# Optimization experiments

Measured on AMD Instinct MI355X. Metric: run time of the kernel, lower is better.

Reference implementation:

```python
import jax, jax.numpy as jnp
import numpy as np

DIM = 256
HEADS = 8
G = 8            # group (window) size per axis
POS_DIM = 16     # (dim // 4) // 4
MLP_HIDDEN = 4 * DIM


def layernorm(x, g, b, eps=1e-5):
    m = x.mean(-1, keepdims=True)
    v = ((x - m) ** 2).mean(-1, keepdims=True)
    return (x - m) / jnp.sqrt(v + eps) * g + b


def setup_inputs() -> dict:
    key = jax.random.key(0)
    ks = jax.random.split(key, 32)
    s = 0.02
    d = {}
    d['x'] = jax.random.normal(ks[0], (1, 32768, DIM), jnp.float32)
    d['y'] = jax.random.normal(ks[1], (1, 32768, DIM), jnp.float32)
    d['n1_g'] = jnp.ones((DIM,), jnp.float32)
    d['n1_b'] = jnp.zeros((DIM,), jnp.float32)
    d['qkv_w'] = jax.random.normal(ks[2], (DIM, 3 * DIM), jnp.float32) * s
    d['qkv_b'] = jnp.zeros((3 * DIM,), jnp.float32)
    d['pp_w'] = jax.random.normal(ks[3], (3, POS_DIM), jnp.float32) * s
    d['pp_b'] = jnp.zeros((POS_DIM,), jnp.float32)
    d['p1_lng'] = jnp.ones((POS_DIM,), jnp.float32)
    d['p1_lnb'] = jnp.zeros((POS_DIM,), jnp.float32)
    d['p1_w'] = jax.random.normal(ks[4], (POS_DIM, POS_DIM), jnp.float32) * s
    d['p1_b'] = jnp.zeros((POS_DIM,), jnp.float32)
    d['p2_lng'] = jnp.ones((POS_DIM,), jnp.float32)
    d['p2_lnb'] = jnp.zeros((POS_DIM,), jnp.float32)
    d['p2_w'] = jax.random.normal(ks[5], (POS_DIM, POS_DIM), jnp.float32) * s
    d['p2_b'] = jnp.zeros((POS_DIM,), jnp.float32)
    d['p3_lng'] = jnp.ones((POS_DIM,), jnp.float32)
    d['p3_lnb'] = jnp.zeros((POS_DIM,), jnp.float32)
    d['p3_w'] = jax.random.normal(ks[6], (POS_DIM, HEADS), jnp.float32) * s
    d['p3_b'] = jnp.zeros((HEADS,), jnp.float32)
    d['proj_w'] = jax.random.normal(ks[7], (DIM, DIM), jnp.float32) * s
    d['proj_b'] = jnp.zeros((DIM,), jnp.float32)
    d['n2_g'] = jnp.ones((DIM,), jnp.float32)
    d['n2_b'] = jnp.zeros((DIM,), jnp.float32)
    d['fc1_w'] = jax.random.normal(ks[8], (DIM, MLP_HIDDEN), jnp.float32) * s
    d['fc1_b'] = jnp.zeros((MLP_HIDDEN,), jnp.float32)
    d['fc2_w'] = jax.random.normal(ks[9], (MLP_HIDDEN, DIM), jnp.float32) * s
    d['fc2_b'] = jnp.zeros((DIM,), jnp.float32)
    d['H'] = 32
    d['W'] = 32
    d['D'] = 32
    return d


def reference(x, y, n1_g, n1_b, qkv_w, qkv_b, pp_w, pp_b,
              p1_lng, p1_lnb, p1_w, p1_b, p2_lng, p2_lnb, p2_w, p2_b,
              p3_lng, p3_lnb, p3_w, p3_b, proj_w, proj_b,
              n2_g, n2_b, fc1_w, fc1_b, fc2_w, fc2_b, H, W, D):
    B, L, C = x.shape
    nh, g = HEADS, G
    hd = C // nh
    shortcut = x
    xn = layernorm(x, n1_g, n1_b)
    xv = xn.reshape(B, H, W, D, C)
    yv = y.reshape(B, H, W, D, C)  # note: y is NOT normed in the original

    # SDA window partition (H,W,D divisible by g -> no padding, zero mask)
    def part(t):
        t = t.reshape(B, H // g, g, W // g, g, D // g, g, C)
        t = t.transpose(0, 1, 3, 5, 2, 4, 6, 7)
        return t.reshape(-1, g * g * g, C)

    xg, yg = part(xv), part(yv)
    B_, N, _ = xg.shape

    # original quirk: self.qkv used for BOTH x and y (qkv_y layer unused)
    qkv = (xg @ qkv_w + qkv_b).reshape(B_, N, 3, nh, hd).transpose(2, 0, 3, 1, 4)
    qkv_y = (yg @ qkv_w + qkv_b).reshape(B_, N, 3, nh, hd).transpose(2, 0, 3, 1, 4)
    q = qkv[0] * (hd ** -0.5)
    k_y, v_y = qkv_y[1], qkv_y[2]

    attn = jnp.einsum('bhnd,bhmd->bhnm', q, k_y)  # [B_, nh, N, N]

    # dynamic relative position bias (small MLP + gather)
    rng = jnp.arange(1 - g, g)
    bh, bw, bd = jnp.meshgrid(rng, rng, rng, indexing='ij')
    biases = jnp.stack([bh, bw, bd], -1).reshape(-1, 3).astype(x.dtype)  # [(2g-1)^3, 3]
    pos = biases @ pp_w + pp_b
    pos = jax.nn.relu(layernorm(pos, p1_lng, p1_lnb)) @ p1_w + p1_b
    pos = jax.nn.relu(layernorm(pos, p2_lng, p2_lnb)) @ p2_w + p2_b
    pos = jax.nn.relu(layernorm(pos, p3_lng, p3_lnb)) @ p3_w + p3_b  # [(2g-1)^3, nh]

    c = jnp.arange(g)
    ch, cw, cd = jnp.meshgrid(c, c, c, indexing='ij')
    cf = jnp.stack([ch, cw, cd], 0).reshape(3, -1)          # [3, g^3]
    rel = (cf[:, :, None] - cf[:, None, :]).transpose(1, 2, 0) + (g - 1)
    idx = rel[..., 0] * (2 * g - 1) * (2 * g - 1) + rel[..., 1] * (2 * g - 1) + rel[..., 2]
    bias = pos[idx].transpose(2, 0, 1)  # [nh, N, N]

    attn = jax.nn.softmax(attn + bias[None], axis=-1)
    out = jnp.einsum('bhnm,bhmd->bhnd', attn, v_y).transpose(0, 2, 1, 3).reshape(B_, N, C)
    out = out @ proj_w + proj_b

    # reverse window partition
    out = out.reshape(B, H // g, W // g, D // g, g, g, g, C)
    out = out.transpose(0, 1, 4, 2, 5, 3, 6, 7).reshape(B, H * W * D, C)

    x = shortcut + out
    x2 = layernorm(x, n2_g, n2_b)
    h = jax.nn.gelu(x2 @ fc1_w + fc1_b, approximate=False)
    x = x + (h @ fc2_w + fc2_b)
    return x
```

## Files before the change

kernel.cpp:

```cpp
#include <hip/hip_runtime.h>
#include <cstdint>
#include <cstddef>

typedef unsigned int u32;
typedef unsigned short u16;
typedef __attribute__((ext_vector_type(8))) short bf16x8;
typedef __attribute__((ext_vector_type(4))) float f32x4;

#define DEV __device__ __forceinline__

DEV u16 f2b(float f){ u32 x = __float_as_uint(f); x += 0x7fffu + ((x>>16)&1u); return (u16)(x>>16); }
DEV u32 pk2(float a, float b){
  u32 r;
  asm("v_cvt_pk_bf16_f32 %0, %1, %2" : "=v"(r) : "v"(a), "v"(b));
  return r;
}

DEV void gll16(const void* g, void* l){
  __builtin_amdgcn_global_load_lds((const __attribute__((address_space(1))) u32*)g,
                                   (__attribute__((address_space(3))) u32*)l, 16, 0, 0);
}

DEV void win_n(int r, int& win, int& n){
  int d_ = r & 31, w_ = (r>>5)&31, h_ = r>>10;
  win = ((h_>>3)<<4) | ((w_>>3)<<2) | (d_>>3);
  n   = ((h_&7)<<6)  | ((w_&7)<<3)  | (d_&7);
}
DEV int tok_of(int r){
  int win = r>>9, nn = r&511;
  int bh = win>>4, bw=(win>>2)&3, bd=win&3;
  int ih = nn>>6,  iw=(nn>>3)&7,  id=nn&7;
  return ((bh*8+ih)<<10) | ((bw*8+iw)<<5) | (bd*8+id);
}


__global__ void wtrall_k(const float* __restrict__ qkv_w, const float* __restrict__ proj_w,
                         const float* __restrict__ fc1_w, const float* __restrict__ fc2_w,
                         u16* __restrict__ qkvT, u16* __restrict__ projT,
                         u16* __restrict__ fc1T, u16* __restrict__ fc2T){
  int f = blockIdx.x*256 + threadIdx.x;
  const float* w; u16* wt; int g; bool k10 = false; int N;
  if (f < 196608)      { w=qkv_w;  wt=qkvT;  g=f;        N=768;  }
  else if (f < 262144) { w=proj_w; wt=projT; g=f-196608; N=256;  }
  else if (f < 524288) { w=fc1_w;  wt=fc1T;  g=f-262144; N=1024; }
  else                 { w=fc2_w;  wt=fc2T;  g=f-524288; N=256;  k10=true; }
  int n = k10 ? (g>>10) : (g>>8);
  int k = k10 ? (g&1023) : (g&255);
  wt[g] = f2b(w[(size_t)k*N + n]);
}

__global__ void conv_k(const float* __restrict__ x, u16* __restrict__ o, int n4){
  int stride = gridDim.x*blockDim.x;
  for (int i = blockIdx.x*blockDim.x + threadIdx.x; i < n4; i += stride){
    const float4 v = *(const float4*)(x + (size_t)i*4);
    u32 lo = (u32)f2b(v.x) | ((u32)f2b(v.y)<<16);
    u32 hi = (u32)f2b(v.z) | ((u32)f2b(v.w)<<16);
    *(uint2*)(o + (size_t)i*4) = make_uint2(lo, hi);
  }
}

__global__ __launch_bounds__(256)
void ln_k(const float* __restrict__ x, const float* __restrict__ g,
          const float* __restrict__ b, u16* __restrict__ out){
  int row  = blockIdx.x*4 + (threadIdx.x>>6);
  int lane = threadIdx.x & 63;
  const float4 v = *(const float4*)(x + (size_t)row*256 + lane*4);
  float s = v.x+v.y+v.z+v.w;
  #pragma unroll
  for (int m=1;m<64;m<<=1) s += __shfl_xor(s, m);
  float mean = s * (1.0f/256.0f);
  float d0=v.x-mean,d1=v.y-mean,d2=v.z-mean,d3=v.w-mean;
  float q = d0*d0+d1*d1+d2*d2+d3*d3;
  #pragma unroll
  for (int m=1;m<64;m<<=1) q += __shfl_xor(q, m);
  float rs = rsqrtf(q*(1.0f/256.0f) + 1e-5f);
  const float4 gg = *(const float4*)(g + lane*4);
  const float4 bb = *(const float4*)(b + lane*4);
  u32 lo = (u32)f2b(d0*rs*gg.x+bb.x) | ((u32)f2b(d1*rs*gg.y+bb.y)<<16);
  u32 hi = (u32)f2b(d2*rs*gg.z+bb.z) | ((u32)f2b(d3*rs*gg.w+bb.w)<<16);
  *(uint2*)(out + (size_t)row*256 + lane*4) = make_uint2(lo,hi);
}

template<int NOUT>
DEV void pstage(float* v, const float* g, const float* b, const float* W, const float* bb){
  float m = 0.f;
  #pragma unroll
  for (int i=0;i<16;i++) m += v[i];
  m *= 0.0625f;
  float q = 0.f;
  #pragma unroll
  for (int i=0;i<16;i++){ float d=v[i]-m; q += d*d; }
  float rs = rsqrtf(q*0.0625f + 1e-5f);
  float u[16];
  #pragma unroll
  for (int i=0;i<16;i++){ float t = (v[i]-m)*rs*g[i] + b[i]; u[i] = t>0.f?t:0.f; }
  #pragma unroll
  for (int o=0;o<NOUT;o++){
    float s = bb[o];
    #pragma unroll
    for (int kk=0;kk<16;kk++) s += u[kk]*W[kk*NOUT+o];
    v[o] = s;
  }
}

__global__ void posmlp_k(const float* pp_w, const float* pp_b,
                         const float* g1, const float* b1, const float* w1, const float* bb1,
                         const float* g2, const float* b2, const float* w2, const float* bb2,
                         const float* g3, const float* b3, const float* w3, const float* bb3,
                         float* __restrict__ posb){
  int i = blockIdx.x*256 + threadIdx.x;
  if (i >= 3375) return;
  int t = i;
  int bd = t % 15; t /= 15;
  int bw = t % 15; t /= 15;
  int bh = t;
  float fh = (float)(bh-7), fw = (float)(bw-7), fd = (float)(bd-7);
  float v[16];
  #pragma unroll
  for (int o=0;o<16;o++) v[o] = fh*pp_w[o] + fw*pp_w[16+o] + fd*pp_w[32+o] + pp_b[o];
  pstage<16>(v, g1,b1,w1,bb1);
  pstage<16>(v, g2,b2,w2,bb2);
  pstage<8> (v, g3,b3,w3,bb3);
  #pragma unroll
  for (int h=0;h<8;h++) posb[(size_t)h*3376 + i] = v[h] * 1.4426950408889634f;
}

struct GemmP {
  const u16* A; const u16* Bt;
  int K;
  const float* bvec;
  float scale;
  const float* add32;
  float* out32;
  u16* out16;
  u16* out16b;
};

template<int MODE>
DEV void epi(const GemmP& p, int r, int c, float val){
  if constexpr (MODE==0){
    float qv = (val + p.bvec[c]) * p.scale;
    int win, n; win_n(r, win, n);
    int hh = c>>5, dd = c&31;
    p.out16[((size_t)((win*8+hh)*512 + n)<<5) + dd] = f2b(qv);
  } else if constexpr (MODE==1){
    float ov = val + p.bvec[c];
    int win, n; win_n(r, win, n);
    int cc = c & 255;
    int hh = cc>>5, dd = cc&31;
    size_t base = (size_t)(win*8+hh)*16384;
    if (c < 256){
      int nc = n>>4, ln2 = ((dd>>3)<<4)|(n&15), jj = dd&7;
      p.out16[base + (size_t)(nc*64+ln2)*8 + jj] = f2b(ov);
    } else {
      int fi = ((n>>5)<<1) | (dd>>4);
      int ln2 = (((n>>3)&3)<<4)|(dd&15), jj = n&7;
      p.out16b[base + (size_t)(fi*64+ln2)*8 + jj] = f2b(ov);
    }
  } else if constexpr (MODE==2){
    int l = tok_of(r);
    size_t o = (size_t)l*256 + c;
    p.out32[o] = val + p.bvec[c] + p.add32[o];
  } else if constexpr (MODE==3){
    float u = val + p.bvec[c];
    float e = exp2f(u*(2.3022083f + 0.1029437f*u*u));
    float ge = u*e*__builtin_amdgcn_rcpf(e+1.f);
    p.out16[(size_t)r*1024 + c] = f2b(ge);
  } else {
    size_t o = (size_t)r*256 + c;
    p.out32[o] = val + p.bvec[c] + p.add32[o];
  }
}

template<int MODE, int NT>
__global__ __launch_bounds__(512, 2)
void gemmA_k(GemmP p){
  __shared__ u16 lA[16384];
  __shared__ u16 lB[3][4096];
  const int tid = threadIdx.x;
  const int wid = tid>>6, lane = tid&63;
  const int lr = lane&15, lg = lane>>4;
  const int m0 = blockIdx.x*64;
  const int wm = (wid>>2)*32, wn = (wid&3)*32;
  const int T = NT*8;
  const f32x4 z4 = {0.f,0.f,0.f,0.f};

  #pragma unroll
  for (int it=0; it<4; ++it){
    int f = it*8 + wid;
    int rt = f>>3, kt = f&7;
    int row = m0 + rt*16 + lr;
    const u16* ga;
    if constexpr (MODE==2){
      ga = p.A + ((size_t)((row>>9)*8 + kt)*512 + (row&511))*32 + lg*8;
    } else {
      ga = p.A + (size_t)row*256 + kt*32 + lg*8;
    }
    gll16(ga, (char*)lA + f*1024 + lane*16);
  }
  auto stageB = [&](int buf, int t){
    int j = t>>3, kt = t&7;
    gll16(p.Bt + (size_t)(j*128 + wid*16 + lr)*256 + kt*32 + lg*8,
          (char*)lB[buf] + wid*1024 + lane*16);
  };
  stageB(0, 0);
  if (T > 1) stageB(1, 1);

  f32x4 acc[2][2];
  #pragma unroll
  for (int i=0;i<2;i++){ acc[i][0]=z4; acc[i][1]=z4; }

  int cur = 0, stg = 2;
  for (int t=0; t<T; ++t){
    const int kt = t&7;
    if (t+1 >= T)          asm volatile("s_waitcnt vmcnt(0)"  ::: "memory");
    else if (kt==0 && t)   asm volatile("s_waitcnt vmcnt(17)" ::: "memory");
    else                   asm volatile("s_waitcnt vmcnt(1)"  ::: "memory");
    __builtin_amdgcn_s_barrier();
    __builtin_amdgcn_sched_barrier(0);
    bf16x8 af[2], bfr[2];
    #pragma unroll
    for (int i=0;i<2;i++){
      int fA = ((wid>>2)*2 + i)*8 + kt;
      af[i] = *(const bf16x8*)((const char*)lA + fA*1024 + lane*16);
    }
    #pragma unroll
    for (int j=0;j<2;j++){
      int fB = (wid&3)*2 + j;
      bfr[j] = *(const bf16x8*)((const char*)lB[cur] + fB*1024 + lane*16);
    }
    #pragma unroll
    for (int i=0;i<2;i++)
      #pragma unroll
      for (int j=0;j<2;j++)
        acc[i][j] = __builtin_amdgcn_mfma_f32_16x16x32_bf16(af[i], bfr[j], acc[i][j], 0,0,0);
    __builtin_amdgcn_sched_barrier(0);
    if (kt == 7){
      int n0 = (t>>3)*128;
      #pragma unroll
      for (int i=0;i<2;i++)
        #pragma unroll
        for (int j=0;j<2;j++){
          #pragma unroll
          for (int v=0;v<4;v++)
            epi<MODE>(p, m0 + wm + i*16 + lg*4 + v, n0 + wn + j*16 + lr, acc[i][j][v]);
          acc[i][j] = z4;
        }
    }
    if (t+2 < T) stageB(stg, t+2);
    cur = (cur==2)?0:cur+1;
    stg = (stg==2)?0:stg+1;
  }
}

__global__ __launch_bounds__(512, 2)
void gemmW_k(GemmP p){
  __shared__ u16 lA[3][2048];
  __shared__ u16 lB[3][8192];
  const int tid = threadIdx.x;
  const int wid = tid>>6, lane = tid&63;
  const int lr = lane&15, lg = lane>>4;
  const int m0 = blockIdx.x*64;
  const int wm = (wid>>2)*32, wn = (wid&3)*64;
  const f32x4 z4 = {0.f,0.f,0.f,0.f};

  auto stage = [&](int buf, int kt){
    {
      int f = wid>>1, half = wid&1;
      if (lane < 32){
        int lg2 = half*2 + (lane>>4);
        gll16(p.A + (size_t)(m0 + f*16 + (lane&15))*1024 + kt*32 + lg2*8,
              (char*)lA[buf] + f*1024 + half*512 + lane*16);
      }
    }
    #pragma unroll
    for (int r=0;r<2;r++){
      int fb = wid*2 + r;
      gll16(p.Bt + (size_t)(fb*16 + lr)*1024 + kt*32 + lg*8,
            (char*)lB[buf] + fb*1024 + lane*16);
    }
  };
  stage(0, 0);
  stage(1, 1);

  f32x4 acc[2][4];
  #pragma unroll
  for (int i=0;i<2;i++)
    #pragma unroll
    for (int j=0;j<4;j++) acc[i][j] = z4;

  int cur = 0, stg = 2;
  for (int kt=0; kt<32; ++kt){
    if (kt+1 < 32) asm volatile("s_waitcnt vmcnt(3)" ::: "memory");
    else           asm volatile("s_waitcnt vmcnt(0)" ::: "memory");
    __builtin_amdgcn_s_barrier();
    __builtin_amdgcn_sched_barrier(0);
    bf16x8 af[2], bfr[4];
    #pragma unroll
    for (int i=0;i<2;i++){
      int fA = (wid>>2)*2 + i;
      af[i] = *(const bf16x8*)((const char*)lA[cur] + fA*1024 + lane*16);
    }
    #pragma unroll
    for (int j=0;j<4;j++){
      int fB = (wid&3)*4 + j;
      bfr[j] = *(const bf16x8*)((const char*)lB[cur] + fB*1024 + lane*16);
    }
    #pragma unroll
    for (int i=0;i<2;i++)
      #pragma unroll
      for (int j=0;j<4;j++)
        acc[i][j] = __builtin_amdgcn_mfma_f32_16x16x32_bf16(af[i], bfr[j], acc[i][j], 0,0,0);
    __builtin_amdgcn_sched_barrier(0);
    if (kt+2 < 32) stage(stg, kt+2);
    cur = (cur==2)?0:cur+1;
    stg = (stg==2)?0:stg+1;
  }

  #pragma unroll
  for (int i=0;i<2;i++)
    #pragma unroll
    for (int j=0;j<4;j++)
      #pragma unroll
      for (int v=0;v<4;v++)
        epi<4>(p, m0 + wm + i*16 + lg*4 + v, wn + j*16 + lr, acc[i][j][v]);
}

__global__ __launch_bounds__(512, 2)
void attn_k(const u16* __restrict__ Q, const u16* __restrict__ Kf,
            const u16* __restrict__ Vf, const float* __restrict__ posb,
            u16* __restrict__ outF){
  __shared__ u16 lK[16384];
  __shared__ u16 lV[16384];
  __shared__ float lPf[3392];
  const int bid = blockIdx.x;
  const int hh = bid&7;
  const int tid = threadIdx.x, wid = tid>>6, lane = tid&63;
  const int lr = lane&15, lg = lane>>4;
  const u16* Kb = Kf + (size_t)bid*16384;
  const u16* Vb = Vf + (size_t)bid*16384;
  const u16* Qb = Q  + (size_t)bid*16384;
  #pragma unroll
  for (int r=0;r<4;r++){
    int off = (r*512 + tid)*16;
    gll16((const char*)Kb + off, (char*)lK + off);
    gll16((const char*)Vb + off, (char*)lV + off);
  }
  const float* ptab = posb + (size_t)hh*3376;
  for (int t=tid; t<3375; t+=512) lPf[t] = ptab[t];
  __syncthreads();
  const f32x4 z4 = {0.f,0.f,0.f,0.f};

  for (int ch=0; ch<4; ++ch){
    const int r0 = wid*64 + ch*16;
    const int q  = r0 + lr;
    const int Ab = (q>>6)*225 + ((q>>3)&7)*15 + (q&7) + 1687 - (lg>>1)*15 - (lg&1)*4;
    bf16x8 qf = *(const bf16x8*)(Qb + (size_t)q*32 + lg*8);
    f32x4 o0 = z4, o1 = z4;
    float sv0 = 0.f, sv1 = 0.f, sv2 = 0.f, sv3 = 0.f;
    #pragma unroll
    for (int ph=0; ph<2; ++ph){
      f32x4 sf[16];
      __builtin_amdgcn_s_setprio(1);
      #pragma unroll
      for (int i=0;i<16;i++){
        int nc = ph*16 + i;
        bf16x8 kf = *(const bf16x8*)&lK[(nc*64 + lane)*8];
        sf[i] = __builtin_amdgcn_mfma_f32_16x16x32_bf16(kf, qf, z4, 0,0,0);
      }
      __builtin_amdgcn_s_setprio(0);
      #pragma unroll
      for (int i=0;i<16;i++){
        int nc = ph*16 + i;
        const float* bp = lPf + (Ab - (nc>>2)*225 - (nc&3)*30 - 3);
        float e3 = exp2f(sf[i][3] + bp[0]);
        float e2 = exp2f(sf[i][2] + bp[1]);
        float e1 = exp2f(sf[i][1] + bp[2]);
        float e0 = exp2f(sf[i][0] + bp[3]);
        sf[i][0]=e0; sf[i][1]=e1; sf[i][2]=e2; sf[i][3]=e3;
        sv0 += e0; sv1 += e1; sv2 += e2; sv3 += e3;
      }
      #pragma unroll
      for (int kc=0;kc<8;kc++){
        u32 a0 = pk2(sf[2*kc  ][0], sf[2*kc  ][1]);
        u32 a1 = pk2(sf[2*kc  ][2], sf[2*kc  ][3]);
        u32 b0 = pk2(sf[2*kc+1][0], sf[2*kc+1][1]);
        u32 b1 = pk2(sf[2*kc+1][2], sf[2*kc+1][3]);
        asm("v_permlane32_swap_b32 %0, %1" : "+v"(a0), "+v"(b0));
        asm("v_permlane16_swap_b32 %0, %1" : "+v"(a0), "+v"(b0));
        asm("v_permlane32_swap_b32 %0, %1" : "+v"(a1), "+v"(b1));
        asm("v_permlane16_swap_b32 %0, %1" : "+v"(a1), "+v"(b1));
        bf16x8 pf;
        ((u32*)&pf)[0]=a0; ((u32*)&pf)[1]=a1; ((u32*)&pf)[2]=b0; ((u32*)&pf)[3]=b1;
        int kcg = ph*8 + kc;
        bf16x8 v0 = *(const bf16x8*)&lV[(size_t)((kcg*2+0)*64 + lane)*8];
        bf16x8 v1 = *(const bf16x8*)&lV[(size_t)((kcg*2+1)*64 + lane)*8];
        __builtin_amdgcn_s_setprio(1);
        o0 = __builtin_amdgcn_mfma_f32_16x16x32_bf16(pf, v0, o0, 0,0,0);
        o1 = __builtin_amdgcn_mfma_f32_16x16x32_bf16(pf, v1, o1, 0,0,0);
        __builtin_amdgcn_s_setprio(0);
      }
    }
    float s = (sv0+sv1) + (sv2+sv3);
    s += __shfl_xor(s,16);
    s += __shfl_xor(s,32);
    #pragma unroll
    for (int v=0;v<4;v++){
      float inv = 1.0f / __shfl(s, lg*4+v);
      int n = r0 + lg*4 + v;
      size_t base = ((size_t)bid*512 + n)*32;
      outF[base + lr]      = f2b(o0[v]*inv);
      outF[base + 16 + lr] = f2b(o1[v]*inv);
    }
  }
}

extern "C" void kernel_launch(void* const* d_in, const int* in_sizes, int n_in,
                              void* d_out, int out_size, void* d_ws, size_t ws_size,
                              hipStream_t stream){
  const float* x      = (const float*)d_in[0];
  const float* y      = (const float*)d_in[1];
  const float* n1_g   = (const float*)d_in[2];
  const float* n1_b   = (const float*)d_in[3];
  const float* qkv_w  = (const float*)d_in[4];
  const float* qkv_b  = (const float*)d_in[5];
  const float* pp_w   = (const float*)d_in[6];
  const float* pp_b   = (const float*)d_in[7];
  const float* p1_lng = (const float*)d_in[8];
  const float* p1_lnb = (const float*)d_in[9];
  const float* p1_w   = (const float*)d_in[10];
  const float* p1_b   = (const float*)d_in[11];
  const float* p2_lng = (const float*)d_in[12];
  const float* p2_lnb = (const float*)d_in[13];
  const float* p2_w   = (const float*)d_in[14];
  const float* p2_b   = (const float*)d_in[15];
  const float* p3_lng = (const float*)d_in[16];
  const float* p3_lnb = (const float*)d_in[17];
  const float* p3_w   = (const float*)d_in[18];
  const float* p3_b   = (const float*)d_in[19];
  const float* proj_w = (const float*)d_in[20];
  const float* proj_b = (const float*)d_in[21];
  const float* n2_g   = (const float*)d_in[22];
  const float* n2_b   = (const float*)d_in[23];
  const float* fc1_w  = (const float*)d_in[24];
  const float* fc1_b  = (const float*)d_in[25];
  const float* fc2_w  = (const float*)d_in[26];
  const float* fc2_b  = (const float*)d_in[27];
  float* out = (float*)d_out;
  char* ws = (char*)d_ws;

  u16*   qkvT  = (u16*)  (ws + 0);
  u16*   projT = (u16*)  (ws + 393216);
  u16*   fc1T  = (u16*)  (ws + 524288);
  u16*   fc2T  = (u16*)  (ws + 1048576);
  float* posb  = (float*)(ws + 1572864);
  u16*   xn    = (u16*)  (ws + 5898240);
  u16*   yb    = (u16*)  (ws + 22675456);
  u16*   Qb    = (u16*)  (ws + 39452672);
  u16*   Kfb   = (u16*)  (ws + 56229888);
  u16*   Vfb   = (u16*)  (ws + 73007104);
  u16*   attnF = (u16*)  (ws + 89784320);
  float* xres  = (float*)(ws + 106561536);
  u16*   hbuf  = xn;
  u16*   x2n   = attnF;

  wtrall_k<<<3072,256,0,stream>>>(qkv_w, proj_w, fc1_w, fc2_w, qkvT, projT, fc1T, fc2T);
  posmlp_k<<<14,256,0,stream>>>(pp_w, pp_b,
                                p1_lng,p1_lnb,p1_w,p1_b,
                                p2_lng,p2_lnb,p2_w,p2_b,
                                p3_lng,p3_lnb,p3_w,p3_b, posb);
  ln_k<<<8192,256,0,stream>>>(x, n1_g, n1_b, xn);
  conv_k<<<2048,256,0,stream>>>(y, yb, 2097152);

  GemmP pq; pq.A=xn; pq.Bt=qkvT; pq.K=256; pq.bvec=qkv_b;
  pq.scale=0.17677669529663687f*1.4426950408889634f;
  pq.add32=nullptr; pq.out32=nullptr; pq.out16=Qb; pq.out16b=nullptr;
  gemmA_k<0,2><<<512,512,0,stream>>>(pq);

  GemmP pkv; pkv.A=yb; pkv.Bt=qkvT + 256*256; pkv.K=256; pkv.bvec=qkv_b + 256;
  pkv.scale=1.f; pkv.add32=nullptr; pkv.out32=nullptr; pkv.out16=Kfb; pkv.out16b=Vfb;
  gemmA_k<1,4><<<512,512,0,stream>>>(pkv);

  attn_k<<<512,512,0,stream>>>(Qb, Kfb, Vfb, posb, attnF);

  GemmP pp; pp.A=attnF; pp.Bt=projT; pp.K=256; pp.bvec=proj_b;
  pp.scale=1.f; pp.add32=x; pp.out32=xres; pp.out16=nullptr; pp.out16b=nullptr;
  gemmA_k<2,2><<<512,512,0,stream>>>(pp);

  ln_k<<<8192,256,0,stream>>>(xres, n2_g, n2_b, x2n);

  GemmP pf1; pf1.A=x2n; pf1.Bt=fc1T; pf1.K=256; pf1.bvec=fc1_b;
  pf1.scale=1.f; pf1.add32=nullptr; pf1.out32=nullptr; pf1.out16=hbuf; pf1.out16b=nullptr;
  gemmA_k<3,8><<<512,512,0,stream>>>(pf1);

  GemmP pf2; pf2.A=hbuf; pf2.Bt=fc2T; pf2.K=1024; pf2.bvec=fc2_b;
  pf2.scale=1.f; pf2.add32=xres; pf2.out32=out; pf2.out16=nullptr; pf2.out16b=nullptr;
  gemmW_k<<<512,512,0,stream>>>(pf2);
}
```

Before: 270.6 us.

## Fuse LayerNorm and bf16 conversion into GEMM A-tile staging; MFMA softmax row sums

Removes the standalone LayerNorm and fp32-to-bf16 conversion kernels by having the QKV, KV and fc1 GEMMs load fp32 activations directly, normalize them in registers and write bf16 into the LDS A tile. This avoids writing and re-reading intermediate bf16 activation buffers and saves three kernel launches. In the attention kernel, softmax denominators now come from an extra MFMA against a vector of ones instead of scalar adds plus cross-lane shuffles. The trade-off is that the fused A-tile load is synchronous register work rather than async global-to-LDS loads, and the row sums are now taken over bf16-rounded probabilities.

Result: faster. 246.7 us (-8.8%).

```diff
diff --git a/kernel.cpp b/kernel.cpp
--- a/kernel.cpp
+++ b/kernel.cpp
@@ -49,38 +49,6 @@
   wt[g] = f2b(w[(size_t)k*N + n]);
 }
 
-__global__ void conv_k(const float* __restrict__ x, u16* __restrict__ o, int n4){
-  int stride = gridDim.x*blockDim.x;
-  for (int i = blockIdx.x*blockDim.x + threadIdx.x; i < n4; i += stride){
-    const float4 v = *(const float4*)(x + (size_t)i*4);
-    u32 lo = (u32)f2b(v.x) | ((u32)f2b(v.y)<<16);
-    u32 hi = (u32)f2b(v.z) | ((u32)f2b(v.w)<<16);
-    *(uint2*)(o + (size_t)i*4) = make_uint2(lo, hi);
-  }
-}
-
-__global__ __launch_bounds__(256)
-void ln_k(const float* __restrict__ x, const float* __restrict__ g,
-          const float* __restrict__ b, u16* __restrict__ out){
-  int row  = blockIdx.x*4 + (threadIdx.x>>6);
-  int lane = threadIdx.x & 63;
-  const float4 v = *(const float4*)(x + (size_t)row*256 + lane*4);
-  float s = v.x+v.y+v.z+v.w;
-  #pragma unroll
-  for (int m=1;m<64;m<<=1) s += __shfl_xor(s, m);
-  float mean = s * (1.0f/256.0f);
-  float d0=v.x-mean,d1=v.y-mean,d2=v.z-mean,d3=v.w-mean;
-  float q = d0*d0+d1*d1+d2*d2+d3*d3;
-  #pragma unroll
-  for (int m=1;m<64;m<<=1) q += __shfl_xor(q, m);
-  float rs = rsqrtf(q*(1.0f/256.0f) + 1e-5f);
-  const float4 gg = *(const float4*)(g + lane*4);
-  const float4 bb = *(const float4*)(b + lane*4);
-  u32 lo = (u32)f2b(d0*rs*gg.x+bb.x) | ((u32)f2b(d1*rs*gg.y+bb.y)<<16);
-  u32 hi = (u32)f2b(d2*rs*gg.z+bb.z) | ((u32)f2b(d3*rs*gg.w+bb.w)<<16);
-  *(uint2*)(out + (size_t)row*256 + lane*4) = make_uint2(lo,hi);
-}
-
 template<int NOUT>
 DEV void pstage(float* v, const float* g, const float* b, const float* W, const float* bb){
   float m = 0.f;
@@ -126,7 +94,10 @@
 }
 
 struct GemmP {
-  const u16* A; const u16* Bt;
+  const u16* A;
+  const float* Af32;
+  const float* lng; const float* lnb;
+  const u16* Bt;
   int K;
   const float* bvec;
   float scale;
@@ -172,7 +143,7 @@
   }
 }
 
-template<int MODE, int NT>
+template<int MODE, int NT, int STG>
 __global__ __launch_bounds__(512, 2)
 void gemmA_k(GemmP p){
   __shared__ u16 lA[16384];
@@ -185,18 +156,56 @@
   const int T = NT*8;
   const f32x4 z4 = {0.f,0.f,0.f,0.f};
 
-  #pragma unroll
-  for (int it=0; it<4; ++it){
-    int f = it*8 + wid;
-    int rt = f>>3, kt = f&7;
-    int row = m0 + rt*16 + lr;
-    const u16* ga;
-    if constexpr (MODE==2){
-      ga = p.A + ((size_t)((row>>9)*8 + kt)*512 + (row&511))*32 + lg*8;
-    } else {
-      ga = p.A + (size_t)row*256 + kt*32 + lg*8;
-    }
-    gll16(ga, (char*)lA + f*1024 + lane*16);
+  if constexpr (STG==3){
+    #pragma unroll
+    for (int it=0; it<4; ++it){
+      int f = it*8 + wid;
+      int rt = f>>3, kt = f&7;
+      int row = m0 + rt*16 + lr;
+      const u16* ga = p.A + ((size_t)((row>>9)*8 + kt)*512 + (row&511))*32 + lg*8;
+      gll16(ga, (char*)lA + f*1024 + lane*16);
+    }
+  } else {
+    const int row = wid*8 + (lane>>3);
+    const int sub = lane&7;
+    const float* src = p.Af32 + (size_t)(m0+row)*256;
+    float xv[32];
+    #pragma unroll
+    for (int j=0;j<8;j++){
+      float4 v = *(const float4*)(src + j*32 + sub*4);
+      xv[j*4+0]=v.x; xv[j*4+1]=v.y; xv[j*4+2]=v.z; xv[j*4+3]=v.w;
+    }
+    float mu=0.f, rs=1.f;
+    if constexpr (STG==1){
+      float s=0.f;
+      #pragma unroll
+      for (int i2=0;i2<32;i2++) s += xv[i2];
+      s += __shfl_xor(s,1); s += __shfl_xor(s,2); s += __shfl_xor(s,4);
+      mu = s*(1.f/256.f);
+      float q2=0.f;
+      #pragma unroll
+      for (int i2=0;i2<32;i2++){ float d=xv[i2]-mu; q2 += d*d; }
+      q2 += __shfl_xor(q2,1); q2 += __shfl_xor(q2,2); q2 += __shfl_xor(q2,4);
+      rs = rsqrtf(q2*(1.f/256.f) + 1e-5f);
+    }
+    const int rt = wid>>1, q = (wid&1)*8 + (lane>>3);
+    #pragma unroll
+    for (int j=0;j<8;j++){
+      float o0,o1,o2,o3;
+      if constexpr (STG==1){
+        float4 gg = *(const float4*)(p.lng + j*32 + sub*4);
+        float4 bb = *(const float4*)(p.lnb + j*32 + sub*4);
+        o0=(xv[j*4+0]-mu)*rs*gg.x+bb.x; o1=(xv[j*4+1]-mu)*rs*gg.y+bb.y;
+        o2=(xv[j*4+2]-mu)*rs*gg.z+bb.z; o3=(xv[j*4+3]-mu)*rs*gg.w+bb.w;
+      } else {
+        o0=xv[j*4+0]; o1=xv[j*4+1]; o2=xv[j*4+2]; o3=xv[j*4+3];
+      }
+      int f = rt*8 + j;
+      *(uint2*)((char*)lA + f*1024 + (sub>>1)*256 + q*16 + (sub&1)*8)
+          = make_uint2((u32)f2b(o0) | ((u32)f2b(o1)<<16),
+                       (u32)f2b(o2) | ((u32)f2b(o3)<<16));
+    }
+    asm volatile("s_waitcnt lgkmcnt(0)" ::: "memory");
   }
   auto stageB = [&](int buf, int t){
     int j = t>>3, kt = t&7;
@@ -350,14 +359,15 @@
   for (int t=tid; t<3375; t+=512) lPf[t] = ptab[t];
   __syncthreads();
   const f32x4 z4 = {0.f,0.f,0.f,0.f};
+  const bf16x8 ones = {(short)0x3F80,(short)0x3F80,(short)0x3F80,(short)0x3F80,
+                       (short)0x3F80,(short)0x3F80,(short)0x3F80,(short)0x3F80};
 
   for (int ch=0; ch<4; ++ch){
     const int r0 = wid*64 + ch*16;
     const int q  = r0 + lr;
     const int Ab = (q>>6)*225 + ((q>>3)&7)*15 + (q&7) + 1687 - (lg>>1)*15 - (lg&1)*4;
     bf16x8 qf = *(const bf16x8*)(Qb + (size_t)q*32 + lg*8);
-    f32x4 o0 = z4, o1 = z4;
-    float sv0 = 0.f, sv1 = 0.f, sv2 = 0.f, sv3 = 0.f;
+    f32x4 o0 = z4, o1 = z4, as_ = z4;
     #pragma unroll
     for (int ph=0; ph<2; ++ph){
       f32x4 sf[16];
@@ -373,12 +383,10 @@
       for (int i=0;i<16;i++){
         int nc = ph*16 + i;
         const float* bp = lPf + (Ab - (nc>>2)*225 - (nc&3)*30 - 3);
-        float e3 = exp2f(sf[i][3] + bp[0]);
-        float e2 = exp2f(sf[i][2] + bp[1]);
-        float e1 = exp2f(sf[i][1] + bp[2]);
-        float e0 = exp2f(sf[i][0] + bp[3]);
-        sf[i][0]=e0; sf[i][1]=e1; sf[i][2]=e2; sf[i][3]=e3;
-        sv0 += e0; sv1 += e1; sv2 += e2; sv3 += e3;
+        sf[i][3] = exp2f(sf[i][3] + bp[0]);
+        sf[i][2] = exp2f(sf[i][2] + bp[1]);
+        sf[i][1] = exp2f(sf[i][1] + bp[2]);
+        sf[i][0] = exp2f(sf[i][0] + bp[3]);
       }
       #pragma unroll
       for (int kc=0;kc<8;kc++){
@@ -396,17 +404,15 @@
         bf16x8 v0 = *(const bf16x8*)&lV[(size_t)((kcg*2+0)*64 + lane)*8];
         bf16x8 v1 = *(const bf16x8*)&lV[(size_t)((kcg*2+1)*64 + lane)*8];
         __builtin_amdgcn_s_setprio(1);
-        o0 = __builtin_amdgcn_mfma_f32_16x16x32_bf16(pf, v0, o0, 0,0,0);
-        o1 = __builtin_amdgcn_mfma_f32_16x16x32_bf16(pf, v1, o1, 0,0,0);
+        o0  = __builtin_amdgcn_mfma_f32_16x16x32_bf16(pf, v0, o0, 0,0,0);
+        o1  = __builtin_amdgcn_mfma_f32_16x16x32_bf16(pf, v1, o1, 0,0,0);
+        as_ = __builtin_amdgcn_mfma_f32_16x16x32_bf16(pf, ones, as_, 0,0,0);
         __builtin_amdgcn_s_setprio(0);
       }
     }
-    float s = (sv0+sv1) + (sv2+sv3);
-    s += __shfl_xor(s,16);
-    s += __shfl_xor(s,32);
     #pragma unroll
     for (int v=0;v<4;v++){
-      float inv = 1.0f / __shfl(s, lg*4+v);
+      float inv = 1.0f / as_[v];
       int n = r0 + lg*4 + v;
       size_t base = ((size_t)bid*512 + n)*32;
       outF[base + lr]      = f2b(o0[v]*inv);
@@ -454,46 +460,44 @@
   u16*   fc1T  = (u16*)  (ws + 524288);
   u16*   fc2T  = (u16*)  (ws + 1048576);
   float* posb  = (float*)(ws + 1572864);
-  u16*   xn    = (u16*)  (ws + 5898240);
-  u16*   yb    = (u16*)  (ws + 22675456);
+  u16*   hbuf  = (u16*)  (ws + 5898240);
   u16*   Qb    = (u16*)  (ws + 39452672);
   u16*   Kfb   = (u16*)  (ws + 56229888);
   u16*   Vfb   = (u16*)  (ws + 73007104);
   u16*   attnF = (u16*)  (ws + 89784320);
   float* xres  = (float*)(ws + 106561536);
-  u16*   hbuf  = xn;
-  u16*   x2n   = attnF;
 
   wtrall_k<<<3072,256,0,stream>>>(qkv_w, proj_w, fc1_w, fc2_w, qkvT, projT, fc1T, fc2T);
   posmlp_k<<<14,256,0,stream>>>(pp_w, pp_b,
                                 p1_lng,p1_lnb,p1_w,p1_b,
                                 p2_lng,p2_lnb,p2_w,p2_b,
                                 p3_lng,p3_lnb,p3_w,p3_b, posb);
-  ln_k<<<8192,256,0,stream>>>(x, n1_g, n1_b, xn);
-  conv_k<<<2048,256,0,stream>>>(y, yb, 2097152);
-
-  GemmP pq; pq.A=xn; pq.Bt=qkvT; pq.K=256; pq.bvec=qkv_b;
+
+  GemmP pq; pq.A=nullptr; pq.Af32=x; pq.lng=n1_g; pq.lnb=n1_b;
+  pq.Bt=qkvT; pq.K=256; pq.bvec=qkv_b;
   pq.scale=0.17677669529663687f*1.4426950408889634f;
   pq.add32=nullptr; pq.out32=nullptr; pq.out16=Qb; pq.out16b=nullptr;
-  gemmA_k<0,2><<<512,512,0,stream>>>(pq);
-
-  GemmP pkv; pkv.A=yb; pkv.Bt=qkvT + 256*256; pkv.K=256; pkv.bvec=qkv_b + 256;
+  gemmA_k<0,2,1><<<512,512,0,stream>>>(pq);
+
+  GemmP pkv; pkv.A=nullptr; pkv.Af32=y; pkv.lng=nullptr; pkv.lnb=nullptr;
+  pkv.Bt=qkvT + 256*256; pkv.K=256; pkv.bvec=qkv_b + 256;
   pkv.scale=1.f; pkv.add32=nullptr; pkv.out32=nullptr; pkv.out16=Kfb; pkv.out16b=Vfb;
-  gemmA_k<1,4><<<512,512,0,stream>>>(pkv);
+  gemmA_k<1,4,2><<<512,512,0,stream>>>(pkv);
 
   attn_k<<<512,512,0,stream>>>(Qb, Kfb, Vfb, posb, attnF);
 
-  GemmP pp; pp.A=attnF; pp.Bt=projT; pp.K=256; pp.bvec=proj_b;
+  GemmP pp; pp.A=attnF; pp.Af32=nullptr; pp.lng=nullptr; pp.lnb=nullptr;
+  pp.Bt=projT; pp.K=256; pp.bvec=proj_b;
   pp.scale=1.f; pp.add32=x; pp.out32=xres; pp.out16=nullptr; pp.out16b=nullptr;
-  gemmA_k<2,2><<<512,512,0,stream>>>(pp);
-
-  ln_k<<<8192,256,0,stream>>>(xres, n2_g, n2_b, x2n);
-
-  GemmP pf1; pf1.A=x2n; pf1.Bt=fc1T; pf1.K=256; pf1.bvec=fc1_b;
+  gemmA_k<2,2,3><<<512,512,0,stream>>>(pp);
+
+  GemmP pf1; pf1.A=nullptr; pf1.Af32=xres; pf1.lng=n2_g; pf1.lnb=n2_b;
+  pf1.Bt=fc1T; pf1.K=256; pf1.bvec=fc1_b;
   pf1.scale=1.f; pf1.add32=nullptr; pf1.out32=nullptr; pf1.out16=hbuf; pf1.out16b=nullptr;
-  gemmA_k<3,8><<<512,512,0,stream>>>(pf1);
-
-  GemmP pf2; pf2.A=hbuf; pf2.Bt=fc2T; pf2.K=1024; pf2.bvec=fc2_b;
+  gemmA_k<3,8,1><<<512,512,0,stream>>>(pf1);
+
+  GemmP pf2; pf2.A=hbuf; pf2.Af32=nullptr; pf2.lng=nullptr; pf2.lnb=nullptr;
+  pf2.Bt=fc2T; pf2.K=1024; pf2.bvec=fc2_b;
   pf2.scale=1.f; pf2.add32=xres; pf2.out32=out; pf2.out16=nullptr; pf2.out16b=nullptr;
   gemmW_k<<<512,512,0,stream>>>(pf2);
 }
```
